# Kernel tuning notes

Hardware: AMD Instinct MI355X
Metric: run time of the kernel (lower is better)

The kernel has to match this reference:

```python
import jax, jax.numpy as jnp
import numpy as np

SCORE_THRESHOLD = 0.5
N = 2_000_000  # flattened anchor grid size
C = 85         # 2 yx + 2 hw + objectness + score + class logits


def setup_inputs() -> dict:
    key = jax.random.key(0)
    k1, k2 = jax.random.split(key)
    inputs = jax.random.uniform(k1, (N, C), dtype=jnp.float32)
    anchors = jax.random.uniform(k2, (N, 4), dtype=jnp.float32)
    return {"inputs": inputs, "anchors": anchors}


def reference(inputs, anchors):
    # Original TF layer compacts rows where score > threshold via boolean
    # indexing (dynamic shape). For a jit-compatible fixed-shape reference we
    # decode all anchors and zero-mask the rows that fail the threshold; the
    # kept rows carry exactly the same decoded values as the TF output.
    cond = inputs[:, 5] > SCORE_THRESHOLD                      # [N]
    pred_yx = inputs[:, :2] * anchors[:, 2:4] + anchors[:, :2]  # [N, 2]
    pred_hw = jnp.exp(inputs[:, 2:4]) * anchors[:, 2:4]         # [N, 2]
    decoded = jnp.concatenate([pred_yx, pred_hw, inputs[:, 4:]], axis=-1)  # [N, C]
    return jnp.where(cond[:, None], decoded, jnp.zeros((), decoded.dtype))
```

## Files before the change

### kernel.cpp

```cpp
#include <hip/hip_runtime.h>


typedef float f4 __attribute__((ext_vector_type(4)));

#define DET_C   85u
#define ROWS    64u
#define ELEMS   (DET_C * ROWS)
#define NF4     (ELEMS / 4u)

__global__ __launch_bounds__(256) void DetectionLayer_kernel(
    const float* __restrict__ in,
    const float* __restrict__ anchors,
    float* __restrict__ out,
    unsigned int N)
{
    __shared__ f4 lds4[NF4];
    __shared__ float cf[ROWS];
    float* ldsf = (float*)lds4;

    const unsigned int tid  = threadIdx.x;
    const unsigned int row0 = blockIdx.x * ROWS;
    const unsigned int nrows = (N - row0 < ROWS) ? (N - row0) : ROWS;

    const size_t ebase = (size_t)row0 * DET_C;
    const f4* in4  = (const f4*)(in  + ebase);
    f4*       out4 = (f4*)(out + ebase);

    if (nrows == ROWS) {
        f4 an;
        if (tid < ROWS)
            an = *(const f4*)(anchors + (size_t)(row0 + tid) * 4u);

#pragma unroll
        for (unsigned int k = 0; k < 5; ++k)
            lds4[tid + k * 256u] = in4[tid + k * 256u];
        if (tid < NF4 - 5u * 256u)
            lds4[tid + 1280u] = in4[tid + 1280u];
        __syncthreads();

        if (tid < ROWS) {
            const unsigned int o = tid * DET_C;
            const float x0 = ldsf[o + 0], x1 = ldsf[o + 1];
            const float x2 = ldsf[o + 2], x3 = ldsf[o + 3];
            cf[tid] = ldsf[o + 5] > 0.5f ? 1.0f : 0.0f;
            ldsf[o + 0] = x0 * an.z + an.x;
            ldsf[o + 1] = x1 * an.w + an.y;
            ldsf[o + 2] = __expf(x2) * an.z;
            ldsf[o + 3] = __expf(x3) * an.w;
        }
        __syncthreads();

#pragma unroll
        for (unsigned int k = 0; k < 6; ++k) {
            const unsigned int i = tid + k * 256u;
            if (k == 5 && i >= NF4) break;
            f4 v = lds4[i];
            const unsigned int e0 = i * 4u;
            const unsigned int rl = e0 / DET_C;
            const unsigned int c0 = e0 - rl * DET_C;
            const float m0 = cf[rl];
            v.x *= m0;
            v.y *= (c0 + 1u >= DET_C) ? cf[rl + 1u] : m0;
            v.z *= (c0 + 2u >= DET_C) ? cf[rl + 1u] : m0;
            v.w *= (c0 + 3u >= DET_C) ? cf[rl + 1u] : m0;
            __builtin_nontemporal_store(v, &out4[i]);
        }
    } else {
        const unsigned int nelem = nrows * DET_C;
        for (unsigned int e = tid; e < nelem; e += 256u) {
            const unsigned int rl = e / DET_C;
            const unsigned int cc = e - rl * DET_C;
            const size_t grow = (size_t)(row0 + rl);
            const float condf = in[grow * DET_C + 5u] > 0.5f ? 1.0f : 0.0f;
            const float val = in[ebase + e];
            const float* ap = anchors + grow * 4u;
            float dec;
            if (cc < 2u)      dec = val * ap[2u + cc] + ap[cc];
            else if (cc < 4u) dec = __expf(val) * ap[cc];
            else              dec = val;
            __builtin_nontemporal_store(dec * condf, &out[ebase + e]);
        }
    }
}

extern "C" void kernel_launch(void* const* d_in, const int* in_sizes, int n_in,
                              void* d_out, int out_size, void* d_ws, size_t ws_size,
                              hipStream_t stream) {
    const float* in      = (const float*)d_in[0];
    const float* anchors = (const float*)d_in[1];
    float* out = (float*)d_out;

    const unsigned int N = (unsigned int)(in_sizes[0] / 85);
    const unsigned int grid = (N + ROWS - 1) / ROWS;

    DetectionLayer_kernel<<<grid, 256, 0, stream>>>(in, anchors, out, N);
}
```

Measured before the change: 249.3 us.

## Use persistent grid-stride blocks with register prefetch of the next chunk

Replaces the one-block-per-64-rows launch with a fixed grid of 2048 persistent blocks, each looping over 32-row chunks. The loads for the next chunk are held in registers while the current chunk is processed out of LDS, so memory reads overlap compute and stores. Anchor decoding is folded into the vectorized output pass, which removes one barrier and the separate per-row decode step. The cost is extra register pressure and more branching per element, and the launch bounds are set to 8 blocks per CU.

```diff
diff --git a/kernel.cpp b/kernel.cpp
--- a/kernel.cpp
+++ b/kernel.cpp
@@ -4,82 +4,113 @@
 typedef float f4 __attribute__((ext_vector_type(4)));
 
 #define DET_C   85u
-#define ROWS    64u
-#define ELEMS   (DET_C * ROWS)
-#define NF4     (ELEMS / 4u)
+#define ROWS    32u
+#define CH_ELEM (DET_C * ROWS)
+#define CH_F4   (CH_ELEM / 4u)
+#define NBLK    2048u
 
-__global__ __launch_bounds__(256) void DetectionLayer_kernel(
+__global__ __launch_bounds__(256, 8) void DetectionLayer_kernel(
     const float* __restrict__ in,
     const float* __restrict__ anchors,
     float* __restrict__ out,
     unsigned int N)
 {
-    __shared__ f4 lds4[NF4];
-    __shared__ float cf[ROWS];
+    __shared__ f4 lds4[CH_F4];
+    __shared__ f4 an_cache[ROWS];
     float* ldsf = (float*)lds4;
 
-    const unsigned int tid  = threadIdx.x;
-    const unsigned int row0 = blockIdx.x * ROWS;
-    const unsigned int nrows = (N - row0 < ROWS) ? (N - row0) : ROWS;
+    const unsigned int tid = threadIdx.x;
+    const unsigned int G   = gridDim.x;
+    const unsigned int nch = N / ROWS;
 
-    const size_t ebase = (size_t)row0 * DET_C;
-    const f4* in4  = (const f4*)(in  + ebase);
-    f4*       out4 = (f4*)(out + ebase);
+    const unsigned int i0 = tid;
+    const unsigned int i1 = tid + 256u;
+    const unsigned int i2 = tid + 512u;
+    const bool has2 = (i2 < CH_F4);
 
-    if (nrows == ROWS) {
-        f4 an;
-        if (tid < ROWS)
-            an = *(const f4*)(anchors + (size_t)(row0 + tid) * 4u);
+    const f4* in4  = (const f4*)in;
+    const f4* anc4 = (const f4*)anchors;
+    f4*       out4 = (f4*)out;
 
-#pragma unroll
-        for (unsigned int k = 0; k < 5; ++k)
-            lds4[tid + k * 256u] = in4[tid + k * 256u];
-        if (tid < NF4 - 5u * 256u)
-            lds4[tid + 1280u] = in4[tid + 1280u];
+    unsigned int c = blockIdx.x;
+    f4 r0, r1, r2, anR;
+
+    if (c < nch) {
+        const f4* p = in4 + (size_t)c * CH_F4;
+        r0 = p[i0];
+        r1 = p[i1];
+        if (has2) r2 = p[i2];
+        if (tid < ROWS) anR = anc4[(size_t)c * ROWS + tid];
+    }
+
+    while (c < nch) {
+        __syncthreads();
+        lds4[i0] = r0;
+        lds4[i1] = r1;
+        if (has2) lds4[i2] = r2;
+        if (tid < ROWS) an_cache[tid] = anR;
         __syncthreads();
 
-        if (tid < ROWS) {
-            const unsigned int o = tid * DET_C;
-            const float x0 = ldsf[o + 0], x1 = ldsf[o + 1];
-            const float x2 = ldsf[o + 2], x3 = ldsf[o + 3];
-            cf[tid] = ldsf[o + 5] > 0.5f ? 1.0f : 0.0f;
-            ldsf[o + 0] = x0 * an.z + an.x;
-            ldsf[o + 1] = x1 * an.w + an.y;
-            ldsf[o + 2] = __expf(x2) * an.z;
-            ldsf[o + 3] = __expf(x3) * an.w;
+        const unsigned int cn = c + G;
+        if (cn < nch) {
+            const f4* p = in4 + (size_t)cn * CH_F4;
+            r0 = p[i0];
+            r1 = p[i1];
+            if (has2) r2 = p[i2];
+            if (tid < ROWS) anR = anc4[(size_t)cn * ROWS + tid];
         }
-        __syncthreads();
 
+        f4* ob = out4 + (size_t)c * CH_F4;
 #pragma unroll
-        for (unsigned int k = 0; k < 6; ++k) {
-            const unsigned int i = tid + k * 256u;
-            if (k == 5 && i >= NF4) break;
+        for (int k = 0; k < 3; ++k) {
+            if (k == 2 && !has2) break;
+            const unsigned int i = (k == 0) ? i0 : (k == 1) ? i1 : i2;
             f4 v = lds4[i];
             const unsigned int e0 = i * 4u;
             const unsigned int rl = e0 / DET_C;
             const unsigned int c0 = e0 - rl * DET_C;
-            const float m0 = cf[rl];
-            v.x *= m0;
-            v.y *= (c0 + 1u >= DET_C) ? cf[rl + 1u] : m0;
-            v.z *= (c0 + 2u >= DET_C) ? cf[rl + 1u] : m0;
-            v.w *= (c0 + 3u >= DET_C) ? cf[rl + 1u] : m0;
-            __builtin_nontemporal_store(v, &out4[i]);
+            if (c0 >= 4u && c0 <= DET_C - 4u) {
+                const float m = ldsf[rl * DET_C + 5u] > 0.5f ? 1.0f : 0.0f;
+                v.x *= m; v.y *= m; v.z *= m; v.w *= m;
+            } else {
+                float vv[4] = {v.x, v.y, v.z, v.w};
+#pragma unroll
+                for (int j = 0; j < 4; ++j) {
+                    unsigned int cc = c0 + (unsigned int)j;
+                    unsigned int rr = rl;
+                    if (cc >= DET_C) { cc -= DET_C; ++rr; }
+                    float d = vv[j];
+                    if (cc < 4u) {
+                        const f4 an = an_cache[rr];
+                        if (cc == 0u)      d = d * an.z + an.x;
+                        else if (cc == 1u) d = d * an.w + an.y;
+                        else if (cc == 2u) d = __expf(d) * an.z;
+                        else               d = __expf(d) * an.w;
+                    }
+                    const float m = ldsf[rr * DET_C + 5u] > 0.5f ? 1.0f : 0.0f;
+                    vv[j] = d * m;
+                }
+                v.x = vv[0]; v.y = vv[1]; v.z = vv[2]; v.w = vv[3];
+            }
+            __builtin_nontemporal_store(v, &ob[i]);
         }
-    } else {
-        const unsigned int nelem = nrows * DET_C;
-        for (unsigned int e = tid; e < nelem; e += 256u) {
-            const unsigned int rl = e / DET_C;
-            const unsigned int cc = e - rl * DET_C;
-            const size_t grow = (size_t)(row0 + rl);
-            const float condf = in[grow * DET_C + 5u] > 0.5f ? 1.0f : 0.0f;
-            const float val = in[ebase + e];
-            const float* ap = anchors + grow * 4u;
-            float dec;
-            if (cc < 2u)      dec = val * ap[2u + cc] + ap[cc];
-            else if (cc < 4u) dec = __expf(val) * ap[cc];
-            else              dec = val;
-            __builtin_nontemporal_store(dec * condf, &out[ebase + e]);
-        }
+        c = cn;
+    }
+
+    const size_t e_start = (size_t)nch * CH_ELEM;
+    const size_t n_elem  = (size_t)N * DET_C;
+    for (size_t e = e_start + (size_t)blockIdx.x * 256u + tid; e < n_elem;
+         e += (size_t)G * 256u) {
+        const size_t rg = e / DET_C;
+        const unsigned int cc = (unsigned int)(e - rg * DET_C);
+        const float condf = in[rg * DET_C + 5u] > 0.5f ? 1.0f : 0.0f;
+        const float val = in[e];
+        const float* ap = anchors + rg * 4u;
+        float dec;
+        if (cc < 2u)      dec = val * ap[2u + cc] + ap[cc];
+        else if (cc < 4u) dec = __expf(val) * ap[cc];
+        else              dec = val;
+        __builtin_nontemporal_store(dec * condf, &out[e]);
     }
 }
 
@@ -90,8 +121,9 @@
     const float* anchors = (const float*)d_in[1];
     float* out = (float*)d_out;
 
-    const unsigned int N = (unsigned int)(in_sizes[0] / 85);
-    const unsigned int grid = (N + ROWS - 1) / ROWS;
+    const unsigned int N   = (unsigned int)(in_sizes[0] / 85);
+    const unsigned int nch = N / ROWS;
+    unsigned int grid = nch < NBLK ? (nch ? nch : 1u) : NBLK;
 
     DetectionLayer_kernel<<<grid, 256, 0, stream>>>(in, anchors, out, N);
 }
```

After: 287.7 us. 1.15x slower.
